# Kernel optimization log

Hardware: AMD Instinct MI355X
Metric: run time of the kernel (lower is better)

Reference implementation:

```python
import jax, jax.numpy as jnp
import numpy as np

N_VERTICES = 24  # hardcoded via torch.eye(24) in the original
K = 3


def normalized_adj(adj):
    # scipy version: L = (A @ D^-1/2).T @ D^-1/2 = D^-1/2 @ A^T @ D^-1/2
    d = adj.sum(axis=1)
    d_inv_sqrt = jnp.where(d > 0, 1.0 / jnp.sqrt(d), 0.0)
    return (adj * d_inv_sqrt[None, :]).T * d_inv_sqrt[None, :]


def cheb_polynomials(L, k_order):
    Ts = [jnp.eye(N_VERTICES, dtype=L.dtype), L]
    for _ in range(2, k_order):
        Ts.append(2.0 * L @ Ts[-1] - Ts[-2])
    return jnp.stack(Ts[:k_order])  # (K, N, N)


def setup_inputs() -> dict:
    key = jax.random.key(0)
    k1, k2, k3 = jax.random.split(key, 3)
    x = jax.random.normal(k1, (64, 32, N_VERTICES, 512), dtype=jnp.float32)
    adj = jax.random.uniform(k2, (N_VERTICES, N_VERTICES), dtype=jnp.float32)
    Theta = jax.random.normal(k3, (K, 32, 32), dtype=jnp.float32)
    return {"x": x, "adj": adj, "Theta": Theta}


def reference(x, adj, Theta):
    # x: (b, c, n, t); adj: (n, n); Theta: (K, c, o)
    L = normalized_adj(adj)
    T = cheb_polynomials(L, K)  # (K, n, m)
    # original per-timestep, per-k: rhs[b,m,c] = sum_n x[b,n,c] T_k[n,m];
    # out[b,m,o] += rhs @ Theta_k. Fused over t and k, final permute -> (b,o,m,t).
    out = jnp.einsum('knm,bcnt,kco->bomt', T, x, Theta)
    return out
```

## Files before the change

### kernel.cpp

```cpp
#include <hip/hip_runtime.h>
#include <hip/hip_bf16.h>
#include <stdint.h>


#define NV 24
#define CIN 32
#define COUT 32
#define TDIM 512
#define BATCH 64
#define MDIM 768
#define KD 768
#define BM 128
#define BN 128
#define BK 32
#define NKT (KD / BK)
#define NTT (TDIM / BN)
#define NMT (MDIM / BM)
#define BLOB (BM * BK)

typedef __attribute__((ext_vector_type(8))) short short8v;
typedef __attribute__((ext_vector_type(4))) float float4v;

__device__ inline unsigned short f2bf(float f) {
    unsigned int u = __float_as_uint(f);
    unsigned int r = (u + 0x7fffu + ((u >> 16) & 1u)) >> 16;
    return (unsigned short)r;
}

__global__ __launch_bounds__(256) void prep_w(const float* __restrict__ adj,
                                              const float* __restrict__ Theta,
                                              unsigned short* __restrict__ Wp) {
    __shared__ float adjS[NV * NV];
    __shared__ float disS[NV];
    __shared__ float LS[NV * NV];
    __shared__ float T2S[NV * NV];
    int tid = threadIdx.x;
    for (int e = tid; e < NV * NV; e += 256) adjS[e] = adj[e];
    __syncthreads();
    if (tid < NV) {
        float d = 0.f;
        for (int j = 0; j < NV; ++j) d += adjS[tid * NV + j];
        disS[tid] = (d > 0.f) ? rsqrtf(d) : 0.f;
    }
    __syncthreads();
    for (int e = tid; e < NV * NV; e += 256) {
        int i = e / NV, j = e % NV;
        LS[e] = disS[i] * adjS[j * NV + i] * disS[j];
    }
    __syncthreads();
    for (int e = tid; e < NV * NV; e += 256) {
        int i = e / NV, j = e % NV;
        float s = 0.f;
        for (int p = 0; p < NV; ++p) s += LS[i * NV + p] * LS[p * NV + j];
        T2S[e] = 2.f * s - (i == j ? 1.f : 0.f);
    }
    __syncthreads();
    int r0 = blockIdx.x * (MDIM / 64);
    for (int e = tid; e < (MDIM / 64) * KD; e += 256) {
        int lr = e / KD, col = e % KD;
        int row = r0 + lr;
        int o = row / NV, m = row % NV;
        int c = col / NV, n = col % NV;
        float th0 = Theta[0 * CIN * COUT + c * COUT + o];
        float th1 = Theta[1 * CIN * COUT + c * COUT + o];
        float th2 = Theta[2 * CIN * COUT + c * COUT + o];
        float v = (n == m ? th0 : 0.f) + LS[n * NV + m] * th1 + T2S[n * NV + m] * th2;
        size_t idx = (((size_t)(row >> 7) * NKT + (col >> 5)) * BM + (row & 127)) * BK + (col & 31);
        Wp[idx] = f2bf(v);
    }
}

__global__ __launch_bounds__(256) void gemm_fused(const unsigned short* __restrict__ Wp,
                                                  const float* __restrict__ x,
                                                  float* __restrict__ out) {
    __shared__ __attribute__((aligned(16))) unsigned short As[BLOB];
    __shared__ __attribute__((aligned(16))) float xF[BK * BN];

    int id = blockIdx.x;
    int hi = id / 48;
    int rem = id - hi * 48;
    int mt = rem >> 3;
    int g = hi * 8 + (rem & 7);
    int b = g >> 2;
    int tt = g & 3;

    int tid = threadIdx.x;
    int wave = tid >> 6;
    int lane = tid & 63;
    int quad = lane >> 4;
    int l16 = lane & 15;
    int wm = wave >> 1, wn = wave & 1;

    const unsigned short* Ab = Wp + (size_t)mt * NKT * BLOB;
    const float* xb = x + (size_t)b * KD * TDIM + tt * BN;

    const float4v zero4 = {0.f, 0.f, 0.f, 0.f};
    float4v acc[4][4];
#pragma unroll
    for (int i = 0; i < 4; ++i)
#pragma unroll
        for (int j = 0; j < 4; ++j) acc[i][j] = zero4;

    for (int kt = 0; kt < NKT; ++kt) {
        __syncthreads();
        const unsigned short* abase = Ab + (size_t)kt * BLOB;
        const float* xrow = xb + (size_t)(kt * BK) * TDIM;
#pragma unroll
        for (int h = 0; h < 2; ++h) {
            const unsigned short* sa = abase + (h * 256 + tid) * 8;
            unsigned short* da = As + (h * 256 + wave * 64) * 8;
            __builtin_amdgcn_global_load_lds(
                (const __attribute__((address_space(1))) void*)sa,
                (__attribute__((address_space(3))) void*)da, 16, 0, 0);
        }
#pragma unroll
        for (int h = 0; h < 4; ++h) {
            int lin = h * 256 + tid;
            int k = lin >> 5;
            int t4 = lin & 31;
            int t4src = t4 ^ ((k >> 3) * 2);
            const float* sx = xrow + (size_t)k * TDIM + t4src * 4;
            float* dx = xF + (h * 1024 + wave * 256);
            __builtin_amdgcn_global_load_lds(
                (const __attribute__((address_space(1))) void*)sx,
                (__attribute__((address_space(3))) void*)dx, 16, 0, 0);
        }
        __syncthreads();

        short8v a[4];
#pragma unroll
        for (int i = 0; i < 4; ++i)
            a[i] = *(const short8v*)(As + (wm * 64 + i * 16 + l16) * BK + quad * 8);

        short8v bb[4];
#pragma unroll
        for (int j = 0; j < 4; ++j) {
            int tloc = wn * 64 + j * 16 + l16;
            int t4 = tloc >> 2, ti = tloc & 3;
            const float* bp = xF + quad * 8 * BN + ((t4 ^ (quad * 2)) << 2) + ti;
            float v0 = bp[0 * BN], v1 = bp[1 * BN], v2 = bp[2 * BN], v3 = bp[3 * BN];
            float v4 = bp[4 * BN], v5 = bp[5 * BN], v6 = bp[6 * BN], v7 = bp[7 * BN];
            union { short8v s; __hip_bfloat162 h[4]; } u;
            u.h[0] = __float22bfloat162_rn({v0, v1});
            u.h[1] = __float22bfloat162_rn({v2, v3});
            u.h[2] = __float22bfloat162_rn({v4, v5});
            u.h[3] = __float22bfloat162_rn({v6, v7});
            bb[j] = u.s;
        }
#pragma unroll
        for (int i = 0; i < 4; ++i)
#pragma unroll
            for (int j = 0; j < 4; ++j)
                acc[i][j] = __builtin_amdgcn_mfma_f32_16x16x32_bf16(a[i], bb[j], acc[i][j], 0, 0, 0);
    }

    float* outB = out + (size_t)b * MDIM * TDIM;
    int rbase = mt * BM + wm * 64;
    int cbase = tt * BN + wn * 64;
#pragma unroll
    for (int i = 0; i < 4; ++i) {
#pragma unroll
        for (int j = 0; j < 4; ++j) {
            int row0 = rbase + i * 16 + quad * 4;
            int col = cbase + j * 16 + l16;
#pragma unroll
            for (int r = 0; r < 4; ++r)
                outB[(size_t)(row0 + r) * TDIM + col] = acc[i][j][r];
        }
    }
}

extern "C" void kernel_launch(void* const* d_in, const int* in_sizes, int n_in,
                              void* d_out, int out_size, void* d_ws, size_t ws_size,
                              hipStream_t stream) {
    const float* x = (const float*)d_in[0];
    const float* adj = (const float*)d_in[1];
    const float* Theta = (const float*)d_in[2];
    float* out = (float*)d_out;

    unsigned short* Wp = (unsigned short*)d_ws;

    prep_w<<<64, 256, 0, stream>>>(adj, Theta, Wp);
    gemm_fused<<<NMT * NTT * BATCH, 256, 0, stream>>>(Wp, x, out);
}
```

Before: 236.7 us.

## Register-prefetch next tile and convert x to bf16 before LDS staging

Replaces the direct global-to-LDS async loads with register prefetching of the next K tile's A and x data, issued after the barrier so the loads overlap the MFMA work on the current tile. x is converted to bf16 once per element when written to LDS, in a transposed, padded layout (stride 40). This lets the B fragments be read as single 16-byte vectors instead of eight scalar float reads plus per-wave conversion. It also sets a launch-bounds occupancy hint of 4 blocks; the cost is higher register pressure and scalar-strided global loads of x.

```diff
diff --git a/kernel.cpp b/kernel.cpp
--- a/kernel.cpp
+++ b/kernel.cpp
@@ -17,6 +17,7 @@
 #define NTT (TDIM / BN)
 #define NMT (MDIM / BM)
 #define BLOB (BM * BK)
+#define BSTRIDE 40
 
 typedef __attribute__((ext_vector_type(8))) short short8v;
 typedef __attribute__((ext_vector_type(4))) float float4v;
@@ -70,11 +71,11 @@
     }
 }
 
-__global__ __launch_bounds__(256) void gemm_fused(const unsigned short* __restrict__ Wp,
-                                                  const float* __restrict__ x,
-                                                  float* __restrict__ out) {
-    __shared__ __attribute__((aligned(16))) unsigned short As[BLOB];
-    __shared__ __attribute__((aligned(16))) float xF[BK * BN];
+__global__ __launch_bounds__(256, 4) void gemm_fused(const unsigned short* __restrict__ Wp,
+                                                     const float* __restrict__ x,
+                                                     float* __restrict__ out) {
+    __shared__ __attribute__((aligned(16))) unsigned short As[BM * BK];
+    __shared__ __attribute__((aligned(16))) unsigned short Bs[BN * BSTRIDE];
 
     int id = blockIdx.x;
     int hi = id / 48;
@@ -90,6 +91,8 @@
     int quad = lane >> 4;
     int l16 = lane & 15;
     int wm = wave >> 1, wn = wave & 1;
+    int kq = wave;
+    int tp = lane;
 
     const unsigned short* Ab = Wp + (size_t)mt * NKT * BLOB;
     const float* xb = x + (size_t)b * KD * TDIM + tt * BN;
@@ -101,52 +104,56 @@
 #pragma unroll
         for (int j = 0; j < 4; ++j) acc[i][j] = zero4;
 
+    uint4 Ar0, Ar1;
+    float Xr[16];
+
+    {
+        const uint4* ap = (const uint4*)Ab;
+        Ar0 = ap[tid];
+        Ar1 = ap[tid + 256];
+        const float* xr = xb + (size_t)(kq * 8) * TDIM;
+#pragma unroll
+        for (int kk = 0; kk < 8; ++kk) {
+            Xr[kk] = xr[(size_t)kk * TDIM + tp];
+            Xr[8 + kk] = xr[(size_t)kk * TDIM + tp + 64];
+        }
+    }
+
     for (int kt = 0; kt < NKT; ++kt) {
+        union { short8v s; __hip_bfloat162 h[4]; } u0, u1;
+#pragma unroll
+        for (int i = 0; i < 4; ++i) {
+            u0.h[i] = __float22bfloat162_rn({Xr[2 * i], Xr[2 * i + 1]});
+            u1.h[i] = __float22bfloat162_rn({Xr[8 + 2 * i], Xr[8 + 2 * i + 1]});
+        }
+        uint4 a0 = Ar0, a1 = Ar1;
+
         __syncthreads();
-        const unsigned short* abase = Ab + (size_t)kt * BLOB;
-        const float* xrow = xb + (size_t)(kt * BK) * TDIM;
-#pragma unroll
-        for (int h = 0; h < 2; ++h) {
-            const unsigned short* sa = abase + (h * 256 + tid) * 8;
-            unsigned short* da = As + (h * 256 + wave * 64) * 8;
-            __builtin_amdgcn_global_load_lds(
-                (const __attribute__((address_space(1))) void*)sa,
-                (__attribute__((address_space(3))) void*)da, 16, 0, 0);
-        }
-#pragma unroll
-        for (int h = 0; h < 4; ++h) {
-            int lin = h * 256 + tid;
-            int k = lin >> 5;
-            int t4 = lin & 31;
-            int t4src = t4 ^ ((k >> 3) * 2);
-            const float* sx = xrow + (size_t)k * TDIM + t4src * 4;
-            float* dx = xF + (h * 1024 + wave * 256);
-            __builtin_amdgcn_global_load_lds(
-                (const __attribute__((address_space(1))) void*)sx,
-                (__attribute__((address_space(3))) void*)dx, 16, 0, 0);
-        }
+        *(uint4*)(As + tid * 8) = a0;
+        *(uint4*)(As + 2048 + tid * 8) = a1;
+        *(short8v*)(Bs + tp * BSTRIDE + kq * 8) = u0.s;
+        *(short8v*)(Bs + (tp + 64) * BSTRIDE + kq * 8) = u1.s;
         __syncthreads();
 
-        short8v a[4];
+        if (kt + 1 < NKT) {
+            const uint4* ap = (const uint4*)(Ab + (size_t)(kt + 1) * BLOB);
+            Ar0 = ap[tid];
+            Ar1 = ap[tid + 256];
+            const float* xr = xb + (size_t)((kt + 1) * BK + kq * 8) * TDIM;
+#pragma unroll
+            for (int kk = 0; kk < 8; ++kk) {
+                Xr[kk] = xr[(size_t)kk * TDIM + tp];
+                Xr[8 + kk] = xr[(size_t)kk * TDIM + tp + 64];
+            }
+        }
+
+        short8v a[4], bb[4];
 #pragma unroll
         for (int i = 0; i < 4; ++i)
             a[i] = *(const short8v*)(As + (wm * 64 + i * 16 + l16) * BK + quad * 8);
-
-        short8v bb[4];
 #pragma unroll
-        for (int j = 0; j < 4; ++j) {
-            int tloc = wn * 64 + j * 16 + l16;
-            int t4 = tloc >> 2, ti = tloc & 3;
-            const float* bp = xF + quad * 8 * BN + ((t4 ^ (quad * 2)) << 2) + ti;
-            float v0 = bp[0 * BN], v1 = bp[1 * BN], v2 = bp[2 * BN], v3 = bp[3 * BN];
-            float v4 = bp[4 * BN], v5 = bp[5 * BN], v6 = bp[6 * BN], v7 = bp[7 * BN];
-            union { short8v s; __hip_bfloat162 h[4]; } u;
-            u.h[0] = __float22bfloat162_rn({v0, v1});
-            u.h[1] = __float22bfloat162_rn({v2, v3});
-            u.h[2] = __float22bfloat162_rn({v4, v5});
-            u.h[3] = __float22bfloat162_rn({v6, v7});
-            bb[j] = u.s;
-        }
+        for (int j = 0; j < 4; ++j)
+            bb[j] = *(const short8v*)(Bs + (wn * 64 + j * 16 + l16) * BSTRIDE + quad * 8);
 #pragma unroll
         for (int i = 0; i < 4; ++i)
 #pragma unroll
```

Result: faster. 221.2 us (-6.5%).
